# Optimization experiments

Hardware: AMD Instinct MI355X
Metric: run time of the kernel (lower is better)

## Reference

```python
import jax, jax.numpy as jnp
import numpy as np

N, S, E, A = 8192, 128, 128, 8  # num_nodes, state_dim, embed_dim, action_dim


def setup_inputs() -> dict:
    key = jax.random.key(0)
    ks = jax.random.split(key, 12)
    sc = lambda d: 1.0 / np.sqrt(d)  # kaiming-ish fan-in scale
    return {
        "state_matrix": jax.random.normal(ks[0], (N, S), dtype=jnp.float32),
        "adj": jax.random.randint(ks[1], (N, N), 0, 2, dtype=jnp.int32),
        # state_mlp: Linear(S,E) -> ReLU -> Linear(E,E)
        "w1": jax.random.normal(ks[2], (S, E), dtype=jnp.float32) * sc(S),
        "b1": jnp.zeros((E,), dtype=jnp.float32),
        "w2": jax.random.normal(ks[3], (E, E), dtype=jnp.float32) * sc(E),
        "b2": jnp.zeros((E,), dtype=jnp.float32),
        # attention projections (no bias)
        "wq": jax.random.normal(ks[4], (E, E), dtype=jnp.float32) * sc(E),
        "wk": jax.random.normal(ks[5], (E, E), dtype=jnp.float32) * sc(E),
        # head: Linear(E,E) -> ReLU -> Linear(E,A)
        "wh1": jax.random.normal(ks[6], (E, E), dtype=jnp.float32) * sc(E),
        "bh1": jnp.zeros((E,), dtype=jnp.float32),
        "wh2": jax.random.normal(ks[7], (E, A), dtype=jnp.float32) * sc(E),
        "bh2": jnp.zeros((A,), dtype=jnp.float32),
    }


def reference(state_matrix, adj, w1, b1, w2, b2, wq, wk, wh1, bh1, wh2, bh2):
    # state_mlp
    h = jnp.maximum(state_matrix @ w1 + b1, 0.0) @ w2 + b2      # [N, E]
    # scaled dot-product attention masked by adjacency
    q = h @ wq                                                   # [N, E]
    k = h @ wk                                                   # [N, E]
    scores = (q @ k.T) * (1.0 / np.sqrt(E))                      # [N, N]
    scores = jnp.where(adj == 0, -jnp.inf, scores)
    attn = jax.nn.softmax(scores, axis=1)                        # [N, N]
    agg = attn @ h                                               # [N, E]
    # output head
    out = jnp.maximum(agg @ wh1 + bh1, 0.0) @ wh2 + bh2          # [N, A]
    return out
```

## Files before the change

kernel.cpp:

```cpp
#include <hip/hip_runtime.h>
#include <hip/hip_bf16.h>
#include <cstdint>

#define NN 8192
#define EE 128
#define AA 8
#define QSCALE 0.08838834764831845f
#define NKVS 8
#define KVLEN (NN / NKVS)
#define NIT (KVLEN / 64)
#define NW (NN / 64)

typedef __attribute__((ext_vector_type(8))) short bf16x8;
typedef __attribute__((ext_vector_type(16))) float f32x16;
typedef unsigned short u16;
typedef unsigned int u32;
typedef unsigned long long u64;

__device__ __forceinline__ u16 bf16_bits(float x) {
    union { float f; u32 u; } v; v.f = x;
    u32 r = v.u + 0x7fffu + ((v.u >> 16) & 1u);
    return (u16)(r >> 16);
}

__device__ __forceinline__ u32 cvtpk_bf16(float lo, float hi) {
    u32 r;
    asm("v_cvt_pk_bf16_f32 %0, %1, %2" : "=v"(r) : "v"(lo), "v"(hi));
    return r;
}

__global__ __launch_bounds__(256) void k_adjmask(
    const int* __restrict__ adj, u64* __restrict__ msk)
{
    const u32 gwave  = (blockIdx.x * 256 + threadIdx.x) >> 6;
    const u32 nwaves = (gridDim.x * 256) >> 6;
    const int lane   = threadIdx.x & 63;
    const size_t nwords = (size_t)NN * NW;
    for (size_t w = (size_t)gwave * 4; w < nwords; w += (size_t)nwaves * 4) {
        u64 b[4];
        #pragma unroll
        for (int u = 0; u < 4; ++u)
            b[u] = __ballot(adj[(w + u) * 64 + lane] != 0);
        if (lane == 0) {
            *reinterpret_cast<ulonglong2*>(&msk[w])     = ulonglong2{b[0], b[1]};
            *reinterpret_cast<ulonglong2*>(&msk[w + 2]) = ulonglong2{b[2], b[3]};
        }
    }
}

__global__ __launch_bounds__(128) void k_mlp(
    const float* __restrict__ state,
    const float* __restrict__ w1, const float* __restrict__ b1,
    const float* __restrict__ w2, const float* __restrict__ b2,
    const float* __restrict__ wq, const float* __restrict__ wk,
    u16* __restrict__ qb, u16* __restrict__ kb, u16* __restrict__ hT)
{
    __shared__ float st[16][EE + 1];
    __shared__ float h1[16][EE + 1];
    const int t  = threadIdx.x;
    const int rg = t >> 4;
    const int ec = (t & 15) * 8;
    const int ra = rg * 2, rb = ra + 1;
    const int r0b = blockIdx.x * 16;

    #pragma unroll
    for (int r = 0; r < 16; ++r)
        st[r][t] = state[(size_t)(r0b + r) * EE + t];
    __syncthreads();

    {
        float a0[8], a1[8];
        #pragma unroll
        for (int j = 0; j < 8; ++j) { float b = b1[ec + j]; a0[j] = b; a1[j] = b; }
        for (int s = 0; s < EE; ++s) {
            float x0 = st[ra][s], x1 = st[rb][s];
            const float* wrow = w1 + s * EE + ec;
            #pragma unroll
            for (int j = 0; j < 8; ++j) { float w = wrow[j]; a0[j] = fmaf(x0, w, a0[j]); a1[j] = fmaf(x1, w, a1[j]); }
        }
        __syncthreads();
        #pragma unroll
        for (int j = 0; j < 8; ++j) { h1[ra][ec + j] = fmaxf(a0[j], 0.f); h1[rb][ec + j] = fmaxf(a1[j], 0.f); }
    }
    __syncthreads();

    float hva[8], hvb[8];
    {
        float a0[8], a1[8];
        #pragma unroll
        for (int j = 0; j < 8; ++j) { float b = b2[ec + j]; a0[j] = b; a1[j] = b; }
        for (int s = 0; s < EE; ++s) {
            float x0 = h1[ra][s], x1 = h1[rb][s];
            const float* wrow = w2 + s * EE + ec;
            #pragma unroll
            for (int j = 0; j < 8; ++j) { float w = wrow[j]; a0[j] = fmaf(x0, w, a0[j]); a1[j] = fmaf(x1, w, a1[j]); }
        }
        #pragma unroll
        for (int j = 0; j < 8; ++j) {
            st[ra][ec + j] = a0[j]; st[rb][ec + j] = a1[j];
            hva[j] = a0[j]; hvb[j] = a1[j];
        }
    }
    __syncthreads();

    {
        float q0[8], q1[8], k0[8], k1[8];
        #pragma unroll
        for (int j = 0; j < 8; ++j) { q0[j] = 0.f; q1[j] = 0.f; k0[j] = 0.f; k1[j] = 0.f; }
        for (int s = 0; s < EE; ++s) {
            float x0 = st[ra][s], x1 = st[rb][s];
            const float* wqr = wq + s * EE + ec;
            const float* wkr = wk + s * EE + ec;
            #pragma unroll
            for (int j = 0; j < 8; ++j) {
                float a = wqr[j], b = wkr[j];
                q0[j] = fmaf(x0, a, q0[j]); q1[j] = fmaf(x1, a, q1[j]);
                k0[j] = fmaf(x0, b, k0[j]); k1[j] = fmaf(x1, b, k1[j]);
            }
        }
        bf16x8 vq0, vq1, vk0, vk1;
        #pragma unroll
        for (int j = 0; j < 8; ++j) {
            vq0[j] = (short)bf16_bits(q0[j] * QSCALE);
            vq1[j] = (short)bf16_bits(q1[j] * QSCALE);
            vk0[j] = (short)bf16_bits(k0[j]);
            vk1[j] = (short)bf16_bits(k1[j]);
        }
        *reinterpret_cast<bf16x8*>(qb + (size_t)(r0b + ra) * EE + ec) = vq0;
        *reinterpret_cast<bf16x8*>(qb + (size_t)(r0b + rb) * EE + ec) = vq1;
        *reinterpret_cast<bf16x8*>(kb + (size_t)(r0b + ra) * EE + ec) = vk0;
        *reinterpret_cast<bf16x8*>(kb + (size_t)(r0b + rb) * EE + ec) = vk1;
    }

    #pragma unroll
    for (int j = 0; j < 8; ++j) {
        u32 pack = (u32)bf16_bits(hva[j]) | ((u32)bf16_bits(hvb[j]) << 16);
        *reinterpret_cast<u32*>(hT + (size_t)(ec + j) * NN + r0b + ra) = pack;
    }
}

__global__ __launch_bounds__(256) void k_attn(
    const u16* __restrict__ qb, const u16* __restrict__ kb,
    const u16* __restrict__ hT, const u64* __restrict__ msk,
    _Float16* __restrict__ pacc, float* __restrict__ pm, float* __restrict__ pl)
{
    __shared__ char smem[65536];

    const int tid  = threadIdx.x;
    const int wv   = tid >> 6;
    const int lane = tid & 63;
    const int l31  = lane & 31;
    const int hf   = lane >> 5;
    const int qt   = blockIdx.x >> 3;
    const int kvs  = blockIdx.x & 7;
    const int qr0  = qt * 128 + wv * 32;
    const int kv0  = kvs * KVLEN;

    bf16x8 qf[8];
    #pragma unroll
    for (int s = 0; s < 8; ++s)
        qf[s] = *reinterpret_cast<const bf16x8*>(
            qb + (size_t)(qr0 + l31) * EE + s * 16 + hf * 8);

    f32x16 acc[4];
    #pragma unroll
    for (int et = 0; et < 4; ++et)
        #pragma unroll
        for (int r = 0; r < 16; ++r) acc[et][r] = 0.f;
    float m = -__builtin_inff(), lsum = 0.f;

    const u64* mrow = msk + (size_t)(qr0 + l31) * NW + kvs * NIT;

    const int kr = tid >> 2, kc = (tid & 3) * 32;
    const int hr = tid >> 1, hc = (tid & 1) * 32;
    const int ksw = (kr & 7) << 4, hsw = (hr & 7) << 4;
    bf16x8 kg[4], hg[4];

    auto LOADG = [&](int c0) {
        #pragma unroll
        for (int u = 0; u < 4; ++u)
            kg[u] = *reinterpret_cast<const bf16x8*>(kb + (size_t)(c0 + kr) * EE + kc + 8 * u);
        #pragma unroll
        for (int u = 0; u < 4; ++u)
            hg[u] = *reinterpret_cast<const bf16x8*>(hT + (size_t)hr * NN + c0 + hc + 8 * u);
    };
    auto WLDS = [&](int b) {
        char* kB = smem + b * 16384;
        #pragma unroll
        for (int u = 0; u < 4; ++u)
            *reinterpret_cast<bf16x8*>(kB + kr * 256 + ((kc * 2 + 16 * u) ^ ksw)) = kg[u];
        char* hB = smem + 32768 + b * 16384;
        #pragma unroll
        for (int u = 0; u < 4; ++u)
            *reinterpret_cast<bf16x8*>(hB + hr * 128 + ((hc * 2 + 16 * u) ^ hsw)) = hg[u];
    };

    LOADG(kv0);
    WLDS(0);
    __syncthreads();

    const int rsw = (l31 & 7) << 4;

    for (int cc = 0; cc < NIT; ++cc) {
        if (cc + 1 < NIT) LOADG(kv0 + (cc + 1) * 64);
        const char* kB = smem + (cc & 1) * 16384;
        const char* hB = smem + 32768 + (cc & 1) * 16384;
        const u64 mw = mrow[cc];

        f32x16 sv0, sv1;
        #pragma unroll
        for (int r = 0; r < 16; ++r) { sv0[r] = 0.f; sv1[r] = 0.f; }
        #pragma unroll
        for (int s = 0; s < 8; ++s) {
            bf16x8 a0 = *reinterpret_cast<const bf16x8*>(
                kB + l31 * 256 + ((s * 32 + hf * 16) ^ rsw));
            sv0 = __builtin_amdgcn_mfma_f32_32x32x16_bf16(a0, qf[s], sv0, 0, 0, 0);
            bf16x8 a1 = *reinterpret_cast<const bf16x8*>(
                kB + (32 + l31) * 256 + ((s * 32 + hf * 16) ^ rsw));
            sv1 = __builtin_amdgcn_mfma_f32_32x32x16_bf16(a1, qf[s], sv1, 0, 0, 0);
        }

        float pv[32];
        float rm = -__builtin_inff();
        #pragma unroll
        for (int r = 0; r < 16; ++r) {
            int k0i = (r & 3) + 8 * (r >> 2) + 4 * hf;
            float v0 = ((mw >> k0i) & 1ull) ? sv0[r] : -__builtin_inff();
            float v1 = ((mw >> (k0i + 32)) & 1ull) ? sv1[r] : -__builtin_inff();
            pv[r] = v0; pv[16 + r] = v1;
            rm = fmaxf(rm, fmaxf(v0, v1));
        }
        rm = fmaxf(rm, __shfl_xor(rm, 32));
        const float mn2 = fmaxf(m, rm);
        const float alpha = (mn2 == m) ? 1.f : __expf(m - mn2);
        m = mn2;

        float rs = 0.f;
        const bool dead = (mn2 == -__builtin_inff());
        #pragma unroll
        for (int i = 0; i < 32; ++i) {
            float p = dead ? 0.f : __expf(pv[i] - mn2);
            pv[i] = p;
            rs += p;
        }
        rs += __shfl_xor(rs, 32);
        lsum = lsum * alpha + rs;

        u32 w[8][2];
        #pragma unroll
        for (int qd = 0; qd < 8; ++qd) {
            int base = 16 * (qd >> 2) + 4 * (qd & 3);
            w[qd][0] = cvtpk_bf16(pv[base], pv[base + 1]);
            w[qd][1] = cvtpk_bf16(pv[base + 2], pv[base + 3]);
        }

        #pragma unroll
        for (int et = 0; et < 4; ++et)
            #pragma unroll
            for (int r = 0; r < 16; ++r) acc[et][r] *= alpha;

        #pragma unroll
        for (int s = 0; s < 4; ++s) {
            u32 s0 = hf == 0 ? w[2 * s + 1][0] : w[2 * s][0];
            u32 s1 = hf == 0 ? w[2 * s + 1][1] : w[2 * s][1];
            u32 r0 = __shfl_xor(s0, 32);
            u32 r1 = __shfl_xor(s1, 32);
            union { u32 u[4]; bf16x8 v; } b2;
            b2.u[0] = hf == 0 ? w[2 * s][0] : r0;
            b2.u[1] = hf == 0 ? w[2 * s][1] : r1;
            b2.u[2] = hf == 0 ? r0 : w[2 * s + 1][0];
            b2.u[3] = hf == 0 ? r1 : w[2 * s + 1][1];
            #pragma unroll
            for (int et = 0; et < 4; ++et) {
                bf16x8 a2 = *reinterpret_cast<const bf16x8*>(
                    hB + (32 * et + l31) * 128 + ((s * 32 + hf * 16) ^ rsw));
                acc[et] = __builtin_amdgcn_mfma_f32_32x32x16_bf16(a2, b2.v, acc[et], 0, 0, 0);
            }
        }
        if (cc + 1 < NIT) WLDS((cc + 1) & 1);
        __syncthreads();
    }

    const size_t pbase = (size_t)kvs * NN + qr0;
    #pragma unroll
    for (int et = 0; et < 4; ++et)
        #pragma unroll
        for (int r = 0; r < 16; ++r) {
            int e = 32 * et + (r & 3) + 8 * (r >> 2) + 4 * hf;
            pacc[(pbase + l31) * EE + e] = (_Float16)acc[et][r];
        }
    if (hf == 0) {
        pm[pbase + l31] = m;
        pl[pbase + l31] = lsum;
    }
}

__global__ __launch_bounds__(256) void k_comb(
    const _Float16* __restrict__ pacc, const float* __restrict__ pm,
    const float* __restrict__ pl, float* __restrict__ agg)
{
    const int row = blockIdx.x * 2 + (threadIdx.x >> 7);
    const int col = threadIdx.x & 127;
    float mp[NKVS], M = -__builtin_inff();
    #pragma unroll
    for (int p = 0; p < NKVS; ++p) { mp[p] = pm[(size_t)p * NN + row]; M = fmaxf(M, mp[p]); }
    float ep[NKVS], L = 0.f;
    #pragma unroll
    for (int p = 0; p < NKVS; ++p) { ep[p] = __expf(mp[p] - M); L += pl[(size_t)p * NN + row] * ep[p]; }
    float s = 0.f;
    #pragma unroll
    for (int p = 0; p < NKVS; ++p)
        s += (float)pacc[((size_t)p * NN + row) * EE + col] * ep[p];
    agg[(size_t)row * EE + col] = s / L;
}

__global__ __launch_bounds__(128) void k_head(
    const float* __restrict__ agg,
    const float* __restrict__ wh1, const float* __restrict__ bh1,
    const float* __restrict__ wh2, const float* __restrict__ bh2,
    float* __restrict__ out)
{
    __shared__ float ag[16][EE + 1];
    __shared__ float h2[16][EE + 1];
    const int t  = threadIdx.x;
    const int rg = t >> 4;
    const int ec = (t & 15) * 8;
    const int ra = rg * 2, rb = ra + 1;
    const int r0b = blockIdx.x * 16;

    #pragma unroll
    for (int r = 0; r < 16; ++r)
        ag[r][t] = agg[(size_t)(r0b + r) * EE + t];
    __syncthreads();
    {
        float a0[8], a1[8];
        #pragma unroll
        for (int j = 0; j < 8; ++j) { float b = bh1[ec + j]; a0[j] = b; a1[j] = b; }
        for (int s = 0; s < EE; ++s) {
            float x0 = ag[ra][s], x1 = ag[rb][s];
            const float* wrow = wh1 + s * EE + ec;
            #pragma unroll
            for (int j = 0; j < 8; ++j) { float w = wrow[j]; a0[j] = fmaf(x0, w, a0[j]); a1[j] = fmaf(x1, w, a1[j]); }
        }
        #pragma unroll
        for (int j = 0; j < 8; ++j) { h2[ra][ec + j] = fmaxf(a0[j], 0.f); h2[rb][ec + j] = fmaxf(a1[j], 0.f); }
    }
    __syncthreads();
    const int r = t >> 3, a = t & 7;
    float o = bh2[a];
    for (int s = 0; s < EE; ++s) o = fmaf(h2[r][s], wh2[s * AA + a], o);
    out[(size_t)(r0b + r) * AA + a] = o;
}

extern "C" void kernel_launch(void* const* d_in, const int* in_sizes, int n_in,
                              void* d_out, int out_size, void* d_ws, size_t ws_size,
                              hipStream_t stream)
{
    (void)in_sizes; (void)n_in; (void)out_size; (void)ws_size;
    const float* state = (const float*)d_in[0];
    const int*   adj   = (const int*)d_in[1];
    const float* w1  = (const float*)d_in[2];
    const float* b1  = (const float*)d_in[3];
    const float* w2  = (const float*)d_in[4];
    const float* b2  = (const float*)d_in[5];
    const float* wq  = (const float*)d_in[6];
    const float* wk  = (const float*)d_in[7];
    const float* wh1 = (const float*)d_in[8];
    const float* bh1 = (const float*)d_in[9];
    const float* wh2 = (const float*)d_in[10];
    const float* bh2 = (const float*)d_in[11];
    float* out = (float*)d_out;

    char* ws = (char*)d_ws;
    const size_t MB = 1024 * 1024;
    u16*      qb   = (u16*)ws;
    u16*      kb   = (u16*)(ws + 2 * MB);
    u16*      hT   = (u16*)(ws + 4 * MB);
    float*    agg  = (float*)(ws + 6 * MB);
    u64*      msk  = (u64*)(ws + 10 * MB);
    _Float16* pacc = (_Float16*)(ws + 18 * MB);
    float*    pm   = (float*)(ws + 34 * MB);
    float*    pl   = (float*)(ws + 34 * MB + 256 * 1024);

    k_mlp    <<<NN / 16, 128, 0, stream>>>(state, w1, b1, w2, b2, wq, wk, qb, kb, hT);
    k_adjmask<<<2048, 256, 0, stream>>>(adj, msk);
    k_attn   <<<(NN / 128) * NKVS, 256, 0, stream>>>(qb, kb, hT, msk, pacc, pm, pl);
    k_comb   <<<NN / 2, 256, 0, stream>>>(pacc, pm, pl, agg);
    k_head   <<<NN / 16, 128, 0, stream>>>(agg, wh1, bh1, wh2, bh2, out);
}
```

Baseline: 197.2 us.

## Fuse adjacency mask and MLP into one launch; enlarge attention query tile

The adjacency bit-packing and the state MLP now run as one kernel, split across disjoint block ranges, with the MLP part using 32-row tiles over 256 threads. The attention kernel moves to 512 threads and 256-query tiles, so each K/H tile staged in LDS is shared by eight waves instead of four, halving K/V global traffic per query. The goal is to drop a launch, let the two preprocessing jobs overlap, and improve reuse. The cost is half as many attention blocks (256 total), which may leave compute units underused, plus register pressure from the launch bound of 512 threads with a minimum of 2 blocks.

```diff
diff --git a/kernel.cpp b/kernel.cpp
--- a/kernel.cpp
+++ b/kernel.cpp
@@ -10,6 +10,7 @@
 #define KVLEN (NN / NKVS)
 #define NIT (KVLEN / 64)
 #define NW (NN / 64)
+#define QTILE 256
 
 typedef __attribute__((ext_vector_type(8))) short bf16x8;
 typedef __attribute__((ext_vector_type(16))) float f32x16;
@@ -29,43 +30,42 @@
     return r;
 }
 
-__global__ __launch_bounds__(256) void k_adjmask(
-    const int* __restrict__ adj, u64* __restrict__ msk)
-{
-    const u32 gwave  = (blockIdx.x * 256 + threadIdx.x) >> 6;
-    const u32 nwaves = (gridDim.x * 256) >> 6;
-    const int lane   = threadIdx.x & 63;
-    const size_t nwords = (size_t)NN * NW;
-    for (size_t w = (size_t)gwave * 4; w < nwords; w += (size_t)nwaves * 4) {
-        u64 b[4];
-        #pragma unroll
-        for (int u = 0; u < 4; ++u)
-            b[u] = __ballot(adj[(w + u) * 64 + lane] != 0);
-        if (lane == 0) {
-            *reinterpret_cast<ulonglong2*>(&msk[w])     = ulonglong2{b[0], b[1]};
-            *reinterpret_cast<ulonglong2*>(&msk[w + 2]) = ulonglong2{b[2], b[3]};
-        }
-    }
-}
-
-__global__ __launch_bounds__(128) void k_mlp(
+__global__ __launch_bounds__(256) void k_pre(
+    const int* __restrict__ adj, u64* __restrict__ msk,
     const float* __restrict__ state,
     const float* __restrict__ w1, const float* __restrict__ b1,
     const float* __restrict__ w2, const float* __restrict__ b2,
     const float* __restrict__ wq, const float* __restrict__ wk,
     u16* __restrict__ qb, u16* __restrict__ kb, u16* __restrict__ hT)
 {
-    __shared__ float st[16][EE + 1];
-    __shared__ float h1[16][EE + 1];
-    const int t  = threadIdx.x;
-    const int rg = t >> 4;
-    const int ec = (t & 15) * 8;
-    const int ra = rg * 2, rb = ra + 1;
-    const int r0b = blockIdx.x * 16;
-
-    #pragma unroll
-    for (int r = 0; r < 16; ++r)
-        st[r][t] = state[(size_t)(r0b + r) * EE + t];
+    __shared__ float st[32][EE + 1];
+    __shared__ float h1[32][EE + 1];
+    const int tid = threadIdx.x;
+
+    if (blockIdx.x < 2048) {
+        const u32 gwave  = (blockIdx.x * 256 + tid) >> 6;
+        const u32 nwaves = (2048 * 256) >> 6;
+        const int lane   = tid & 63;
+        const size_t nwords = (size_t)NN * NW;
+        for (size_t w = (size_t)gwave * 4; w < nwords; w += (size_t)nwaves * 4) {
+            u64 b[4];
+            #pragma unroll
+            for (int u = 0; u < 4; ++u)
+                b[u] = __ballot(adj[(w + u) * 64 + lane] != 0);
+            if (lane == 0) {
+                *reinterpret_cast<ulonglong2*>(&msk[w])     = ulonglong2{b[0], b[1]};
+                *reinterpret_cast<ulonglong2*>(&msk[w + 2]) = ulonglong2{b[2], b[3]};
+            }
+        }
+        return;
+    }
+
+    const int r0b = (blockIdx.x - 2048) * 32;
+    const int ec  = (tid & 15) * 8;
+    const int ra  = (tid >> 4) * 2, rb = ra + 1;
+
+    for (int i = tid; i < 32 * EE; i += 256)
+        st[i >> 7][i & 127] = state[(size_t)r0b * EE + i];
     __syncthreads();
 
     {
@@ -139,7 +139,7 @@
     }
 }
 
-__global__ __launch_bounds__(256) void k_attn(
+__global__ __launch_bounds__(512, 2) void k_attn(
     const u16* __restrict__ qb, const u16* __restrict__ kb,
     const u16* __restrict__ hT, const u64* __restrict__ msk,
     _Float16* __restrict__ pacc, float* __restrict__ pm, float* __restrict__ pl)
@@ -153,7 +153,7 @@
     const int hf   = lane >> 5;
     const int qt   = blockIdx.x >> 3;
     const int kvs  = blockIdx.x & 7;
-    const int qr0  = qt * 128 + wv * 32;
+    const int qr0  = qt * QTILE + wv * 32;
     const int kv0  = kvs * KVLEN;
 
     bf16x8 qf[8];
@@ -171,28 +171,24 @@
 
     const u64* mrow = msk + (size_t)(qr0 + l31) * NW + kvs * NIT;
 
-    const int kr = tid >> 2, kc = (tid & 3) * 32;
-    const int hr = tid >> 1, hc = (tid & 1) * 32;
+    const int kr = tid >> 3, kc = (tid & 7) * 16;
+    const int hr = tid >> 2, hc = (tid & 3) * 16;
     const int ksw = (kr & 7) << 4, hsw = (hr & 7) << 4;
-    bf16x8 kg[4], hg[4];
+    bf16x8 kg[2], hg[2];
 
     auto LOADG = [&](int c0) {
-        #pragma unroll
-        for (int u = 0; u < 4; ++u)
-            kg[u] = *reinterpret_cast<const bf16x8*>(kb + (size_t)(c0 + kr) * EE + kc + 8 * u);
-        #pragma unroll
-        for (int u = 0; u < 4; ++u)
-            hg[u] = *reinterpret_cast<const bf16x8*>(hT + (size_t)hr * NN + c0 + hc + 8 * u);
+        kg[0] = *reinterpret_cast<const bf16x8*>(kb + (size_t)(c0 + kr) * EE + kc);
+        kg[1] = *reinterpret_cast<const bf16x8*>(kb + (size_t)(c0 + kr) * EE + kc + 8);
+        hg[0] = *reinterpret_cast<const bf16x8*>(hT + (size_t)hr * NN + c0 + hc);
+        hg[1] = *reinterpret_cast<const bf16x8*>(hT + (size_t)hr * NN + c0 + hc + 8);
     };
     auto WLDS = [&](int b) {
         char* kB = smem + b * 16384;
-        #pragma unroll
-        for (int u = 0; u < 4; ++u)
-            *reinterpret_cast<bf16x8*>(kB + kr * 256 + ((kc * 2 + 16 * u) ^ ksw)) = kg[u];
+        *reinterpret_cast<bf16x8*>(kB + kr * 256 + ((kc * 2) ^ ksw))      = kg[0];
+        *reinterpret_cast<bf16x8*>(kB + kr * 256 + ((kc * 2 + 16) ^ ksw)) = kg[1];
         char* hB = smem + 32768 + b * 16384;
-        #pragma unroll
-        for (int u = 0; u < 4; ++u)
-            *reinterpret_cast<bf16x8*>(hB + hr * 128 + ((hc * 2 + 16 * u) ^ hsw)) = hg[u];
+        *reinterpret_cast<bf16x8*>(hB + hr * 128 + ((hc * 2) ^ hsw))      = hg[0];
+        *reinterpret_cast<bf16x8*>(hB + hr * 128 + ((hc * 2 + 16) ^ hsw)) = hg[1];
     };
 
     LOADG(kv0);
@@ -323,9 +319,8 @@
     __shared__ float ag[16][EE + 1];
     __shared__ float h2[16][EE + 1];
     const int t  = threadIdx.x;
-    const int rg = t >> 4;
     const int ec = (t & 15) * 8;
-    const int ra = rg * 2, rb = ra + 1;
+    const int ra = (t >> 4) * 2, rb = ra + 1;
     const int r0b = blockIdx.x * 16;
 
     #pragma unroll
@@ -382,9 +377,9 @@
     float*    pm   = (float*)(ws + 34 * MB);
     float*    pl   = (float*)(ws + 34 * MB + 256 * 1024);
 
-    k_mlp    <<<NN / 16, 128, 0, stream>>>(state, w1, b1, w2, b2, wq, wk, qb, kb, hT);
-    k_adjmask<<<2048, 256, 0, stream>>>(adj, msk);
-    k_attn   <<<(NN / 128) * NKVS, 256, 0, stream>>>(qb, kb, hT, msk, pacc, pm, pl);
-    k_comb   <<<NN / 2, 256, 0, stream>>>(pacc, pm, pl, agg);
-    k_head   <<<NN / 16, 128, 0, stream>>>(agg, wh1, bh1, wh2, bh2, out);
-}
+    k_pre  <<<2048 + NN / 32, 256, 0, stream>>>(adj, msk, state, w1, b1, w2, b2,
+                                                wq, wk, qb, kb, hT);
+    k_attn <<<(NN / QTILE) * NKVS, 512, 0, stream>>>(qb, kb, hT, msk, pacc, pm, pl);
+    k_comb <<<NN / 2, 256, 0, stream>>>(pacc, pm, pl, agg);
+    k_head <<<NN / 16, 128, 0, stream>>>(agg, wh1, bh1, wh2, bh2, out);
+}
```

Measured after the change: 224.9 us. 14.0% more time.

## Double attention query tile to 256 rows with 512-thread blocks sharing K/V tiles

Applied to the files above, without the earlier changes.

The attention kernel now runs 8 waves per block, covering 256 query rows instead of 128, so each K and hT tile staged in shared memory serves twice as many query rows. Global-to-LDS traffic per query row is halved, and each thread loads half as many vectors per iteration. The trade-off is half as many blocks (256 instead of 512) and a 64KB LDS footprint per block, which may limit occupancy and wave scheduling. The launch_bounds(512,2) hint also constrains register allocation.

```diff
diff --git a/kernel.cpp b/kernel.cpp
--- a/kernel.cpp
+++ b/kernel.cpp
@@ -10,6 +10,7 @@
 #define KVLEN (NN / NKVS)
 #define NIT (KVLEN / 64)
 #define NW (NN / 64)
+#define QTILE 256
 
 typedef __attribute__((ext_vector_type(8))) short bf16x8;
 typedef __attribute__((ext_vector_type(16))) float f32x16;
@@ -58,9 +59,8 @@
     __shared__ float st[16][EE + 1];
     __shared__ float h1[16][EE + 1];
     const int t  = threadIdx.x;
-    const int rg = t >> 4;
     const int ec = (t & 15) * 8;
-    const int ra = rg * 2, rb = ra + 1;
+    const int ra = (t >> 4) * 2, rb = ra + 1;
     const int r0b = blockIdx.x * 16;
 
     #pragma unroll
@@ -139,7 +139,7 @@
     }
 }
 
-__global__ __launch_bounds__(256) void k_attn(
+__global__ __launch_bounds__(512, 2) void k_attn(
     const u16* __restrict__ qb, const u16* __restrict__ kb,
     const u16* __restrict__ hT, const u64* __restrict__ msk,
     _Float16* __restrict__ pacc, float* __restrict__ pm, float* __restrict__ pl)
@@ -153,7 +153,7 @@
     const int hf   = lane >> 5;
     const int qt   = blockIdx.x >> 3;
     const int kvs  = blockIdx.x & 7;
-    const int qr0  = qt * 128 + wv * 32;
+    const int qr0  = qt * QTILE + wv * 32;
     const int kv0  = kvs * KVLEN;
 
     bf16x8 qf[8];
@@ -171,28 +171,24 @@
 
     const u64* mrow = msk + (size_t)(qr0 + l31) * NW + kvs * NIT;
 
-    const int kr = tid >> 2, kc = (tid & 3) * 32;
-    const int hr = tid >> 1, hc = (tid & 1) * 32;
+    const int kr = tid >> 3, kc = (tid & 7) * 16;
+    const int hr = tid >> 2, hc = (tid & 3) * 16;
     const int ksw = (kr & 7) << 4, hsw = (hr & 7) << 4;
-    bf16x8 kg[4], hg[4];
+    bf16x8 kg[2], hg[2];
 
     auto LOADG = [&](int c0) {
-        #pragma unroll
-        for (int u = 0; u < 4; ++u)
-            kg[u] = *reinterpret_cast<const bf16x8*>(kb + (size_t)(c0 + kr) * EE + kc + 8 * u);
-        #pragma unroll
-        for (int u = 0; u < 4; ++u)
-            hg[u] = *reinterpret_cast<const bf16x8*>(hT + (size_t)hr * NN + c0 + hc + 8 * u);
+        kg[0] = *reinterpret_cast<const bf16x8*>(kb + (size_t)(c0 + kr) * EE + kc);
+        kg[1] = *reinterpret_cast<const bf16x8*>(kb + (size_t)(c0 + kr) * EE + kc + 8);
+        hg[0] = *reinterpret_cast<const bf16x8*>(hT + (size_t)hr * NN + c0 + hc);
+        hg[1] = *reinterpret_cast<const bf16x8*>(hT + (size_t)hr * NN + c0 + hc + 8);
     };
     auto WLDS = [&](int b) {
         char* kB = smem + b * 16384;
-        #pragma unroll
-        for (int u = 0; u < 4; ++u)
-            *reinterpret_cast<bf16x8*>(kB + kr * 256 + ((kc * 2 + 16 * u) ^ ksw)) = kg[u];
+        *reinterpret_cast<bf16x8*>(kB + kr * 256 + ((kc * 2) ^ ksw))      = kg[0];
+        *reinterpret_cast<bf16x8*>(kB + kr * 256 + ((kc * 2 + 16) ^ ksw)) = kg[1];
         char* hB = smem + 32768 + b * 16384;
-        #pragma unroll
-        for (int u = 0; u < 4; ++u)
-            *reinterpret_cast<bf16x8*>(hB + hr * 128 + ((hc * 2 + 16 * u) ^ hsw)) = hg[u];
+        *reinterpret_cast<bf16x8*>(hB + hr * 128 + ((hc * 2) ^ hsw))      = hg[0];
+        *reinterpret_cast<bf16x8*>(hB + hr * 128 + ((hc * 2 + 16) ^ hsw)) = hg[1];
     };
 
     LOADG(kv0);
@@ -323,9 +319,8 @@
     __shared__ float ag[16][EE + 1];
     __shared__ float h2[16][EE + 1];
     const int t  = threadIdx.x;
-    const int rg = t >> 4;
     const int ec = (t & 15) * 8;
-    const int ra = rg * 2, rb = ra + 1;
+    const int ra = (t >> 4) * 2, rb = ra + 1;
     const int r0b = blockIdx.x * 16;
 
     #pragma unroll
@@ -384,7 +379,7 @@
 
     k_mlp    <<<NN / 16, 128, 0, stream>>>(state, w1, b1, w2, b2, wq, wk, qb, kb, hT);
     k_adjmask<<<2048, 256, 0, stream>>>(adj, msk);
-    k_attn   <<<(NN / 128) * NKVS, 256, 0, stream>>>(qb, kb, hT, msk, pacc, pm, pl);
+    k_attn   <<<(NN / QTILE) * NKVS, 512, 0, stream>>>(qb, kb, hT, msk, pacc, pm, pl);
     k_comb   <<<NN / 2, 256, 0, stream>>>(pacc, pm, pl, agg);
     k_head   <<<NN / 16, 128, 0, stream>>>(agg, wh1, bh1, wh2, bh2, out);
 }
```

After: 180.2 us. 8.6% less time.
